# Kernel optimization log

Hardware: AMD Instinct MI355X
Metric: run time of the kernel (lower is better)

## Reference

```python
import jax, jax.numpy as jnp
import numpy as np

B, S, H = 4, 128, 768
OUT, TAG = 24, 4


def setup_inputs() -> dict:
    key = jax.random.key(0)
    k1, k2, k3, k4, k5 = jax.random.split(key, 5)
    x = jax.random.normal(k1, (B, S, H), dtype=jnp.float32)
    # linear1: in 2H -> out 3H ; linear2: in 3H -> out TAG*OUT
    s1 = 1.0 / np.sqrt(2 * H)
    s2 = 1.0 / np.sqrt(3 * H)
    W1 = jax.random.uniform(k2, (2 * H, 3 * H), minval=-s1, maxval=s1, dtype=jnp.float32)
    b1 = jax.random.uniform(k3, (3 * H,), minval=-s1, maxval=s1, dtype=jnp.float32)
    W2 = jax.random.uniform(k4, (3 * H, TAG * OUT), minval=-s2, maxval=s2, dtype=jnp.float32)
    b2 = jax.random.uniform(k5, (TAG * OUT,), minval=-s2, maxval=s2, dtype=jnp.float32)
    return {"x": x, "W1": W1, "b1": b1, "W2": W2, "b2": b2}


def reference(x, W1, b1, W2, b2):
    b, s, h = x.shape
    # pairs[b,i,j] = concat(x[b,i], x[b,j]); avoid explicit 2H concat by
    # splitting W1 into head/tail halves (same math as cat -> linear1).
    W1h, W1t = W1[:h], W1[h:]
    head = jnp.einsum('bih,hk->bik', x, W1h)          # [B,S,3H]
    tail = jnp.einsum('bjh,hk->bjk', x, W1t)          # [B,S,3H]
    hid = head[:, :, None, :] + tail[:, None, :, :] + b1  # [B,S,S,3H]
    hid = jax.nn.relu(hid)  # dropout is identity in eval mode
    scores = jnp.einsum('bijk,ko->bijo', hid, W2) + b2     # [B,S,S,TAG*OUT]
    return scores.reshape(b, s, s, OUT, TAG)
```

## Files before the change

### kernel.cpp

```cpp
#include <hip/hip_runtime.h>
#include <hip/hip_bf16.h>


typedef __bf16 bf16x8 __attribute__((ext_vector_type(8)));
typedef _Float16 f16x8 __attribute__((ext_vector_type(8)));
typedef float f32x4 __attribute__((ext_vector_type(4)));

#define S_   128
#define H_   768
#define K3   2304
#define NOUT 96
#define NIT  36

__device__ __forceinline__ unsigned short f2bf(float f) {
    union { __bf16 b; unsigned short u; } c;
    c.b = (__bf16)f;
    return c.u;
}

__device__ __forceinline__ unsigned short f2h(float f) {
    union { _Float16 h; unsigned short u; } c;
    c.h = (_Float16)f;
    return c.u;
}

__device__ __forceinline__ void gload_lds16(const unsigned short* g, unsigned short* l) {
    __builtin_amdgcn_global_load_lds(
        (const __attribute__((address_space(1))) void*)g,
        (__attribute__((address_space(3))) void*)l,
        16, 0, 0);
}

__global__ __launch_bounds__(256) void k_prep(
        const float* __restrict__ x, unsigned short* __restrict__ xb,
        const float* __restrict__ W1, unsigned short* __restrict__ w1t,
        const float* __restrict__ W2, unsigned short* __restrict__ w2f) {
    __shared__ float tile[32][33];
    const int bid = blockIdx.x, tid = threadIdx.x;
    if (bid < 384) {
        int t = bid * 256 + tid;
        float4 v = ((const float4*)x)[t];
        ushort4 o;
        o.x = f2bf(v.x); o.y = f2bf(v.y); o.z = f2bf(v.z); o.w = f2bf(v.w);
        ((ushort4*)xb)[t] = o;
    } else if (bid < 3840) {
        int idx = bid - 384;
        int bx = idx % 72, by = (idx / 72) % 24, bz = idx / 1728;
        const float* src = W1 + (size_t)bz * H_ * K3;
        unsigned short* dst = w1t + (size_t)bz * K3 * H_;
        int c0 = bx * 32, r0 = by * 32;
        int row = tid >> 3, c4 = (tid & 7) * 4;
        float4 v = *(const float4*)(src + (size_t)(r0 + row) * K3 + c0 + c4);
        tile[row][c4 + 0] = v.x; tile[row][c4 + 1] = v.y;
        tile[row][c4 + 2] = v.z; tile[row][c4 + 3] = v.w;
        __syncthreads();
        ushort4 o;
        o.x = f2bf(tile[c4 + 0][row]); o.y = f2bf(tile[c4 + 1][row]);
        o.z = f2bf(tile[c4 + 2][row]); o.w = f2bf(tile[c4 + 3][row]);
        *(ushort4*)(dst + (size_t)(c0 + row) * H_ + r0 + c4) = o;
    } else {
        int t = (bid - 3840) * 256 + tid;
        int l = t & 63, f = (t >> 6) % 6, kc = t / 384;
        int k0 = kc * 32 + (l >> 4) * 8;
        int o  = f * 16 + (l & 15);
        unsigned short v[8];
#pragma unroll
        for (int e = 0; e < 8; e++)
            v[e] = f2h(W2[(size_t)(k0 + e) * NOUT + o]);
        *(uint4*)(w2f + (size_t)t * 8) = *(const uint4*)v;
    }
}

__global__ __launch_bounds__(256) void k_gemm1(
        const unsigned short* __restrict__ xb,
        const unsigned short* __restrict__ w1t,
        const float* __restrict__ b1,
        unsigned short* __restrict__ headh,
        unsigned short* __restrict__ tailsw) {
    __shared__ unsigned short As[64 * 32];
    __shared__ unsigned short Bs[128 * 32];
    const int tid = threadIdx.x;
    const int l = tid & 63, w = tid >> 6;
    const int m0 = blockIdx.y * 64;
    const int n0 = blockIdx.x * 128;
    const int wr = (w >> 1) * 32, wc = (w & 1) * 64;
    const int lr = l & 15, lk = (l >> 4) * 8;
    f32x4 acc[2][4] = {};

    for (int kt = 0; kt < H_; kt += 32) {
        {
            int row = tid >> 2, seg = (tid & 3) * 8;
            gload_lds16(xb + (size_t)(m0 + row) * H_ + kt + seg, As + tid * 8);
        }
#pragma unroll
        for (int p = 0; p < 2; ++p) {
            int idx = p * 256 + tid;
            int row = idx >> 2, seg = (idx & 3) * 8;
            gload_lds16(w1t + (size_t)(n0 + row) * H_ + kt + seg, Bs + idx * 8);
        }
        asm volatile("s_waitcnt vmcnt(0)" ::: "memory");
        __syncthreads();
        bf16x8 af[2], bfr[4];
#pragma unroll
        for (int i = 0; i < 2; i++) af[i]  = *(const bf16x8*)(As + (wr + i * 16 + lr) * 32 + lk);
#pragma unroll
        for (int j = 0; j < 4; j++) bfr[j] = *(const bf16x8*)(Bs + (wc + j * 16 + lr) * 32 + lk);
#pragma unroll
        for (int i = 0; i < 2; i++)
#pragma unroll
            for (int j = 0; j < 4; j++)
                acc[i][j] = __builtin_amdgcn_mfma_f32_16x16x32_bf16(af[i], bfr[j], acc[i][j], 0, 0, 0);
        __syncthreads();
    }

    const bool tailblk = (n0 >= K3);
    const int nloc = n0 - (tailblk ? K3 : 0);
    const int lv = (l >> 4) * 4;
    if (!tailblk) {
#pragma unroll
        for (int j = 0; j < 4; j++) {
            int c = nloc + wc + j * 16 + lr;
#pragma unroll
            for (int i = 0; i < 2; i++) {
                int mrow = m0 + wr + i * 16 + lv;
#pragma unroll
                for (int e = 0; e < 4; e++)
                    headh[(size_t)(mrow + e) * K3 + c] = f2h(acc[i][j][e]);
            }
        }
    } else {
#pragma unroll
        for (int j = 0; j < 4; j++) {
            int c = nloc + wc + j * 16 + lr;
            float bias = b1[c];
            int chunk = c >> 6, kin = c & 63, u = kin >> 3, ee = kin & 7;
#pragma unroll
            for (int i = 0; i < 2; i++) {
                int mrow = m0 + wr + i * 16 + lv;
#pragma unroll
                for (int e = 0; e < 4; e++) {
                    int r = mrow + e;
                    int jbg = r >> 4, rr = r & 15;
                    size_t idx = (((size_t)(jbg * 36 + chunk) * 8 + u) * 16 + rr) * 8 + ee;
                    tailsw[idx] = f2h(acc[i][j][e] + bias);
                }
            }
        }
    }
}

__device__ __forceinline__ f16x8 form8t(uint4 hq, f16x8 t) {
    union { uint4 q; f16x8 v; } H;
    H.q = hq;
    f16x8 s = H.v + t;
    const f16x8 z = {0, 0, 0, 0, 0, 0, 0, 0};
    return __builtin_elementwise_max(s, z);
}

__global__ __launch_bounds__(256) void k_pair(
        const unsigned short* __restrict__ headh,
        const unsigned short* __restrict__ tailsw,
        const unsigned short* __restrict__ w2f,
        const float* __restrict__ b2,
        float* __restrict__ out) {
    __shared__ __align__(16) unsigned short wlds[4][6144];
    __shared__ __align__(16) unsigned short tlds[4][1024];

    const int tid = threadIdx.x;
    const int w = tid >> 6, l = tid & 63;
    const int lr = l & 15, lkq = l >> 4;
    const int lkoff = lkq * 8;
    const int jb = blockIdx.x;
    const int ig = blockIdx.y;
    const int b  = blockIdx.z;
    const int i0 = ig * 8;

    const unsigned short* Hp   = headh + (size_t)(b * S_ + i0 + 2 * w) * K3;
    const unsigned short* Tsrc = tailsw + (size_t)(b * 8 + jb) * 36 * 1024;

    f32x4 acc[2][6] = {};
    float b2v[6];
#pragma unroll
    for (int f = 0; f < 6; f++) b2v[f] = b2[f * 16 + lr];

    auto stage = [&](int sbuf, int c) {
        const unsigned short* wsrc = w2f + (size_t)c * 6144;
#pragma unroll
        for (int i = 0; i < 3; ++i)
            gload_lds16(wsrc + i * 2048 + tid * 8, &wlds[sbuf][i * 2048 + tid * 8]);
        const unsigned short* tsrc = Tsrc + (size_t)c * 1024;
#pragma unroll
        for (int h = 0; h < 2; ++h)
            gload_lds16(tsrc + h * 512 + l * 8, &tlds[sbuf][h * 512 + l * 8]);
    };

    stage(0, 0);
    stage(1, 1);
    uint4 ha[2], hb[2];
#pragma unroll
    for (int kk = 0; kk < 2; kk++) {
        ha[kk] = *(const uint4*)(Hp + kk * 32 + lkoff);
        hb[kk] = *(const uint4*)(Hp + K3 + kk * 32 + lkoff);
    }

    for (int n = 0; n < NIT; ++n) {
        stage((n + 2) & 3, (n + 2 < NIT) ? (n + 2) : (NIT - 1));
        const int kn = ((n < NIT - 1) ? (n + 1) : n) * 64;
        uint4 han[2], hbn[2];
#pragma unroll
        for (int kk = 0; kk < 2; kk++) {
            han[kk] = *(const uint4*)(Hp + kn + kk * 32 + lkoff);
            hbn[kk] = *(const uint4*)(Hp + K3 + kn + kk * 32 + lkoff);
        }

        asm volatile("s_waitcnt vmcnt(9)" ::: "memory");
        __builtin_amdgcn_s_barrier();

        const unsigned short* Lb = &wlds[n & 3][0];
        const unsigned short* Tb = &tlds[n & 3][0];
        __builtin_amdgcn_s_setprio(1);
#pragma unroll
        for (int kk = 0; kk < 2; kk++) {
            f16x8 t8 = *(const f16x8*)(Tb + (kk * 4 + lkq) * 128 + lr * 8);
            f16x8 a0 = form8t(ha[kk], t8);
            f16x8 a1 = form8t(hb[kk], t8);
#pragma unroll
            for (int f = 0; f < 6; f++) {
                f16x8 bfr = *(const f16x8*)(Lb + kk * 3072 + f * 512 + l * 8);
                acc[0][f] = __builtin_amdgcn_mfma_f32_16x16x32_f16(a0, bfr, acc[0][f], 0, 0, 0);
                acc[1][f] = __builtin_amdgcn_mfma_f32_16x16x32_f16(a1, bfr, acc[1][f], 0, 0, 0);
            }
        }
        __builtin_amdgcn_s_setprio(0);
#pragma unroll
        for (int kk = 0; kk < 2; kk++) { ha[kk] = han[kk]; hb[kk] = hbn[kk]; }
    }

    float* O = out + (((size_t)(b * S_ + i0 + 2 * w)) * S_ + jb * 16) * NOUT;
#pragma unroll
    for (int q = 0; q < 2; q++)
#pragma unroll
        for (int f = 0; f < 6; f++)
#pragma unroll
            for (int e = 0; e < 4; e++) {
                int j = lkq * 4 + e;
                O[(size_t)q * S_ * NOUT + (size_t)j * NOUT + f * 16 + lr] = acc[q][f][e] + b2v[f];
            }
}

extern "C" void kernel_launch(void* const* d_in, const int* in_sizes, int n_in,
                              void* d_out, int out_size, void* d_ws, size_t ws_size,
                              hipStream_t stream) {
    const float* x  = (const float*)d_in[0];
    const float* W1 = (const float*)d_in[1];
    const float* b1 = (const float*)d_in[2];
    const float* W2 = (const float*)d_in[3];
    const float* b2 = (const float*)d_in[4];
    float* out = (float*)d_out;

    char* ws = (char*)d_ws;
    unsigned short* xb     = (unsigned short*)(ws);
    unsigned short* w1t    = (unsigned short*)(ws +   786432);
    unsigned short* w2f    = (unsigned short*)(ws +  7864320);
    unsigned short* headh  = (unsigned short*)(ws +  8306688);
    unsigned short* tailsw = (unsigned short*)(ws + 10665984);

    hipLaunchKernelGGL(k_prep, dim3(3948), dim3(256), 0, stream,
                       x, xb, W1, w1t, W2, w2f);
    hipLaunchKernelGGL(k_gemm1, dim3(36, 8), dim3(256), 0, stream,
                       xb, w1t, b1, headh, tailsw);
    hipLaunchKernelGGL(k_pair, dim3(8, 16, 4), dim3(256), 0, stream,
                       headh, tailsw, w2f, b2, out);
}
```

Baseline: 61.29 us.

## Triple-buffer gemm1 LDS staging and phase-align pair kernel LDS reads with MFMA

The first GEMM now prefetches its x and W1 tiles two stages ahead into a three-deep LDS ring. A single barrier per iteration replaces the full vmcnt(0) drain and the two syncthreads, so global loads overlap the MFMA work. In the pairwise scoring kernel, all six W2 fragments are read from LDS before the MFMAs, and extra barriers are added so waves alternate between a load phase and a compute phase, with setprio around the MFMA block. The extra barriers and registers could add stalls or lower occupancy instead of improving overlap.

Result: no change. 61.64 us (+0.6%).

```diff
diff --git a/kernel.cpp b/kernel.cpp
--- a/kernel.cpp
+++ b/kernel.cpp
@@ -77,8 +77,7 @@
         const float* __restrict__ b1,
         unsigned short* __restrict__ headh,
         unsigned short* __restrict__ tailsw) {
-    __shared__ unsigned short As[64 * 32];
-    __shared__ unsigned short Bs[128 * 32];
+    __shared__ __align__(16) unsigned short AB[3][6144];
     const int tid = threadIdx.x;
     const int l = tid & 63, w = tid >> 6;
     const int m0 = blockIdx.y * 64;
@@ -86,31 +85,42 @@
     const int wr = (w >> 1) * 32, wc = (w & 1) * 64;
     const int lr = l & 15, lk = (l >> 4) * 8;
     f32x4 acc[2][4] = {};
-
-    for (int kt = 0; kt < H_; kt += 32) {
+    const int NKT = H_ / 32;
+
+    auto stage = [&](int sbuf, int kt) {
         {
             int row = tid >> 2, seg = (tid & 3) * 8;
-            gload_lds16(xb + (size_t)(m0 + row) * H_ + kt + seg, As + tid * 8);
+            gload_lds16(xb + (size_t)(m0 + row) * H_ + kt * 32 + seg, &AB[sbuf][tid * 8]);
         }
 #pragma unroll
         for (int p = 0; p < 2; ++p) {
             int idx = p * 256 + tid;
             int row = idx >> 2, seg = (idx & 3) * 8;
-            gload_lds16(w1t + (size_t)(n0 + row) * H_ + kt + seg, Bs + idx * 8);
-        }
-        asm volatile("s_waitcnt vmcnt(0)" ::: "memory");
-        __syncthreads();
+            gload_lds16(w1t + (size_t)(n0 + row) * H_ + kt * 32 + seg,
+                        &AB[sbuf][2048 + idx * 8]);
+        }
+    };
+
+    stage(0, 0);
+    stage(1, 1);
+
+    for (int n = 0; n < NKT; ++n) {
+        asm volatile("s_waitcnt vmcnt(3)" ::: "memory");
+        __builtin_amdgcn_s_barrier();
+        stage((n + 2) % 3, (n + 2 < NKT) ? (n + 2) : (NKT - 1));
+
+        const unsigned short* Ab = &AB[n % 3][0];
+        const unsigned short* Bb = &AB[n % 3][2048];
         bf16x8 af[2], bfr[4];
 #pragma unroll
-        for (int i = 0; i < 2; i++) af[i]  = *(const bf16x8*)(As + (wr + i * 16 + lr) * 32 + lk);
-#pragma unroll
-        for (int j = 0; j < 4; j++) bfr[j] = *(const bf16x8*)(Bs + (wc + j * 16 + lr) * 32 + lk);
+        for (int i = 0; i < 2; i++) af[i]  = *(const bf16x8*)(Ab + (wr + i * 16 + lr) * 32 + lk);
+#pragma unroll
+        for (int j = 0; j < 4; j++) bfr[j] = *(const bf16x8*)(Bb + (wc + j * 16 + lr) * 32 + lk);
 #pragma unroll
         for (int i = 0; i < 2; i++)
 #pragma unroll
             for (int j = 0; j < 4; j++)
                 acc[i][j] = __builtin_amdgcn_mfma_f32_16x16x32_bf16(af[i], bfr[j], acc[i][j], 0, 0, 0);
-        __syncthreads();
     }
 
     const bool tailblk = (n0 >= K3);
@@ -212,26 +222,30 @@
             han[kk] = *(const uint4*)(Hp + kn + kk * 32 + lkoff);
             hbn[kk] = *(const uint4*)(Hp + K3 + kn + kk * 32 + lkoff);
         }
-
         asm volatile("s_waitcnt vmcnt(9)" ::: "memory");
         __builtin_amdgcn_s_barrier();
 
         const unsigned short* Lb = &wlds[n & 3][0];
         const unsigned short* Tb = &tlds[n & 3][0];
-        __builtin_amdgcn_s_setprio(1);
 #pragma unroll
         for (int kk = 0; kk < 2; kk++) {
             f16x8 t8 = *(const f16x8*)(Tb + (kk * 4 + lkq) * 128 + lr * 8);
+            f16x8 bfr[6];
+#pragma unroll
+            for (int f = 0; f < 6; f++)
+                bfr[f] = *(const f16x8*)(Lb + kk * 3072 + f * 512 + l * 8);
+            __builtin_amdgcn_s_barrier();
             f16x8 a0 = form8t(ha[kk], t8);
             f16x8 a1 = form8t(hb[kk], t8);
+            __builtin_amdgcn_s_setprio(1);
 #pragma unroll
             for (int f = 0; f < 6; f++) {
-                f16x8 bfr = *(const f16x8*)(Lb + kk * 3072 + f * 512 + l * 8);
-                acc[0][f] = __builtin_amdgcn_mfma_f32_16x16x32_f16(a0, bfr, acc[0][f], 0, 0, 0);
-                acc[1][f] = __builtin_amdgcn_mfma_f32_16x16x32_f16(a1, bfr, acc[1][f], 0, 0, 0);
-            }
-        }
-        __builtin_amdgcn_s_setprio(0);
+                acc[0][f] = __builtin_amdgcn_mfma_f32_16x16x32_f16(a0, bfr[f], acc[0][f], 0, 0, 0);
+                acc[1][f] = __builtin_amdgcn_mfma_f32_16x16x32_f16(a1, bfr[f], acc[1][f], 0, 0, 0);
+            }
+            __builtin_amdgcn_s_setprio(0);
+            if (kk == 0) __builtin_amdgcn_s_barrier();
+        }
 #pragma unroll
         for (int kk = 0; kk < 2; kk++) { ha[kk] = han[kk]; hb[kk] = hbn[kk]; }
     }
```
